# Kernel tuning notes

Measured on AMD Instinct MI355X. Metric: run time of the kernel, lower is better.

## Reference

```python
import jax, jax.numpy as jnp
import numpy as np

V = 100000
E = 524288
D_IN = 128
D_OUT = 128
NUM_REL = 474
BN_EPS = 1e-5


def setup_inputs() -> dict:
    key = jax.random.key(0)
    ks = jax.random.split(key, 12)
    return {
        "x": jax.random.normal(ks[0], (V, D_IN), dtype=jnp.float32),
        "rel_repr": jax.random.normal(ks[1], (NUM_REL, D_IN), dtype=jnp.float32),
        "edge_norm": jax.random.uniform(ks[2], (E,), dtype=jnp.float32),
        "in_w": jax.random.normal(ks[3], (D_IN, D_OUT), dtype=jnp.float32) * 0.1,
        "out_w": jax.random.normal(ks[4], (D_IN, D_OUT), dtype=jnp.float32) * 0.1,
        "loop_w": jax.random.normal(ks[5], (D_IN, D_OUT), dtype=jnp.float32) * 0.1,
        "w_rel": jax.random.normal(ks[6], (D_IN, D_OUT), dtype=jnp.float32) * 0.1,
        "loop_rel": jax.random.normal(ks[7], (1, D_IN), dtype=jnp.float32),
        "bias": jnp.zeros((D_OUT,), dtype=jnp.float32),
        "src": jax.random.randint(ks[8], (E,), 0, V, dtype=jnp.int32),
        "dst": jax.random.randint(ks[9], (E,), 0, V, dtype=jnp.int32),
        "edge_type": jax.random.randint(ks[10], (E,), 0, NUM_REL, dtype=jnp.int32),
    }


def reference(x, rel_repr, edge_norm, in_w, out_w, loop_w, w_rel, loop_rel, bias, src, dst, edge_type):
    # comp primitive 'mult': edge_data = src_emb * rel[edge_type]   [E, D_IN]
    rel = rel_repr  # num_base=-1 -> rel_wt is None, rel.data = rel_repr
    edge_data = x[src] * rel[edge_type]
    half = edge_data.shape[0] // 2  # static under jit
    # first half of edges -> in_w, second half -> out_w
    msg = jnp.concatenate([edge_data[:half] @ in_w, edge_data[half:] @ out_w], axis=0)
    msg = msg * edge_norm[:, None]
    # agg primitive 'sum': scatter-sum into dst nodes
    agg = jax.ops.segment_sum(msg, dst, num_segments=x.shape[0])  # [V, D_OUT]
    # self-loop path: comp(x, loop_rel) @ loop_w
    loop_msg = (x * loop_rel) @ loop_w
    # comb primitive 'add', scaled by 1/3 (dropout with p=0 is identity)
    h = (agg + loop_msg) * (1.0 / 3.0)
    h = h + bias
    # BatchNorm1d, training-mode batch stats, gamma=1, beta=0
    mean = jnp.mean(h, axis=0)
    var = jnp.mean((h - mean) ** 2, axis=0)
    h = (h - mean) * jax.lax.rsqrt(var + BN_EPS)
    # act primitive 'relu'; ltr=True -> project relations
    return jax.nn.relu(h), rel @ w_rel
```

## Files before the change

### kernel.cpp

```cpp
#include <hip/hip_runtime.h>

#define V 100000
#define VP 100096
#define E_EDGES 524288
#define HALF 262144
#define D 128
#define NREL 474
#define BN_EPS 1e-5f
#define NBLK 98

#define ROWTILES 782
#define GEMM_GRID 1568
#define RED_BLKS 98
#define RELB 237
#define BNBLK 12500

#define LDK 392
#define LDB 40

typedef unsigned short u16;
typedef unsigned int u32;
typedef unsigned long long u64;
typedef __attribute__((ext_vector_type(8))) short short8;
typedef __attribute__((ext_vector_type(4))) float f32x4;

__device__ __forceinline__ u16 f2bf(float f) {
    union { float f; u32 u; } v; v.f = f;
    u32 u = v.u;
    return (u16)((u + 0x7fffu + ((u >> 16) & 1u)) >> 16);
}
__device__ __forceinline__ u32 pk2(float a, float b) {
    return (u32)f2bf(a) | ((u32)f2bf(b) << 16);
}

__global__ __launch_bounds__(256) void hist_k(const int* __restrict__ dst, u32* __restrict__ cnt) {
    int e = blockIdx.x * 256 + threadIdx.x;
    if (e >= E_EDGES) return;
    u32 d = (u32)dst[e];
    if (d >= V) d = 0;
    atomicAdd(&cnt[d], 1u);
}

__global__ __launch_bounds__(1024) void scanA_k(const u32* __restrict__ cnt,
                                                u32* __restrict__ cursor,
                                                u32* __restrict__ bsum) {
    __shared__ u32 wsum[16];
    int tid = threadIdx.x, wid = tid >> 6, lane = tid & 63;
    int idx = blockIdx.x * 1024 + tid;
    u32 v = (idx < V) ? cnt[idx] : 0u;
    u32 s = v;
#pragma unroll
    for (int o = 1; o < 64; o <<= 1) {
        u32 t = __shfl_up(s, o, 64);
        if (lane >= o) s += t;
    }
    if (lane == 63) wsum[wid] = s;
    __syncthreads();
    if (wid == 0) {
        u32 wv = (lane < 16) ? wsum[lane] : 0u;
#pragma unroll
        for (int o = 1; o < 16; o <<= 1) {
            u32 t = __shfl_up(wv, o, 64);
            if (lane >= o) wv += t;
        }
        if (lane < 16) wsum[lane] = wv;
    }
    __syncthreads();
    u32 wprev = wid ? wsum[wid - 1] : 0u;
    if (idx < V) cursor[idx] = s + wprev - v;
    if (tid == 0) bsum[blockIdx.x] = wsum[15];
}

__global__ __launch_bounds__(128) void scanBbt_k(
    u32* __restrict__ bsum,
    const float* __restrict__ in_w, const float* __restrict__ out_w,
    const float* __restrict__ loop_w, u16* __restrict__ Bt) {
    if (blockIdx.x > 0) {
        int n = blockIdx.x - 1;
        int t = threadIdx.x;
        const float* Ws[3] = {in_w, out_w, loop_w};
#pragma unroll
        for (int seg = 0; seg < 3; seg++)
            Bt[(size_t)n * 384 + seg * 128 + t] = f2bf(Ws[seg][(size_t)t * D + n]);
        return;
    }
    __shared__ u32 wtot;
    int t = threadIdx.x, lane = t & 63, w = t >> 6;
    u32 v = (t < NBLK) ? bsum[t] : 0u;
    u32 s = v;
#pragma unroll
    for (int o = 1; o < 64; o <<= 1) {
        u32 x = __shfl_up(s, o, 64);
        if (lane >= o) s += x;
    }
    if (w == 0 && lane == 63) wtot = s;
    __syncthreads();
    u32 add = (w == 1) ? wtot : 0u;
    if (t < NBLK) bsum[t] = add + s - v;
}

__global__ __launch_bounds__(256) void fill_rec_k(
    const int* __restrict__ dst, const int* __restrict__ src, const int* __restrict__ etype,
    const float* __restrict__ enorm, u32* __restrict__ cursor, const u32* __restrict__ bsum,
    u64* __restrict__ rec) {
    int e = blockIdx.x * 256 + threadIdx.x;
    if (e >= E_EDGES) return;
    u32 d = (u32)dst[e];   if (d >= V) d = 0;
    u32 s = (u32)src[e];   if (s >= V) s = 0;
    u32 t = (u32)etype[e]; if (t >= NREL) t = 0;
    float nm = enorm[e];
    u32 w = s | (t << 17) | ((e < HALF ? 0u : 1u) << 26);
    u32 slot = atomicAdd(&cursor[d], 1u) + bsum[d >> 10];
    u64 r = (u64)w | ((u64)__float_as_uint(nm) << 32);
    if (slot < E_EDGES) rec[slot] = r;
}

struct Rec { u32 s, t, hf; float nm; };
__device__ __forceinline__ Rec dec(u64 r) {
    Rec q; u32 w = (u32)r;
    q.s = w & 0x1FFFFu;
    q.t = (w >> 17) & 0x1FFu;
    q.hf = (w >> 26) & 1u;
    q.nm = __uint_as_float((u32)(r >> 32));
    return q;
}

__global__ __launch_bounds__(256) void gather_k(
    const float* __restrict__ x, const float* __restrict__ rel,
    const u32* __restrict__ cursor, const u32* __restrict__ cnt,
    const u32* __restrict__ bsum, const u64* __restrict__ rec, u16* __restrict__ Aagg) {
    int tid = threadIdx.x;
    int wave = tid >> 6, lane = tid & 63;
    int l32 = lane & 31;
    int v = blockIdx.x * 8 + wave * 2 + (lane >> 5);
    int col = l32 * 4;

    u32 n = 0, end = 0;
    if (v < V) {
        n = cnt[v];
        end = cursor[v] + bsum[v >> 10];
        if (end > E_EDGES) end = E_EDGES;
        if (n > end) n = end;
    }
    u32 p = end - n;
    u32 rounds = (n + 3) >> 2;
    u32 ro = (u32)__shfl_xor((int)rounds, 32);
    u32 rw = rounds > ro ? rounds : ro;

    float iA0=0.f,iA1=0.f,iA2=0.f,iA3=0.f, oA0=0.f,oA1=0.f,oA2=0.f,oA3=0.f;
    float iB0=0.f,iB1=0.f,iB2=0.f,iB3=0.f, oB0=0.f,oB1=0.f,oB2=0.f,oB3=0.f;

    for (u32 r = 0; r < rw; r++) {
        u32 q = p + r * 4;
        u32 i0 = (q     < end) ? q     : (u32)E_EDGES;
        u32 i1 = (q + 1 < end) ? q + 1 : (u32)E_EDGES;
        u32 i2 = (q + 2 < end) ? q + 2 : (u32)E_EDGES;
        u32 i3 = (q + 3 < end) ? q + 3 : (u32)E_EDGES;
        u64 r0 = rec[i0], r1 = rec[i1], r2 = rec[i2], r3 = rec[i3];
        Rec q0 = dec(r0), q1 = dec(r1), q2 = dec(r2), q3 = dec(r3);
        float4 x0 = *(const float4*)(x + (size_t)q0.s * D + col);
        float4 x1 = *(const float4*)(x + (size_t)q1.s * D + col);
        float4 x2 = *(const float4*)(x + (size_t)q2.s * D + col);
        float4 x3 = *(const float4*)(x + (size_t)q3.s * D + col);
        float4 v0 = *(const float4*)(rel + (size_t)q0.t * D + col);
        float4 v1 = *(const float4*)(rel + (size_t)q1.t * D + col);
        float4 v2 = *(const float4*)(rel + (size_t)q2.t * D + col);
        float4 v3 = *(const float4*)(rel + (size_t)q3.t * D + col);
        float f00 = x0.x*v0.x*q0.nm, f01 = x0.y*v0.y*q0.nm, f02 = x0.z*v0.z*q0.nm, f03 = x0.w*v0.w*q0.nm;
        float f10 = x1.x*v1.x*q1.nm, f11 = x1.y*v1.y*q1.nm, f12 = x1.z*v1.z*q1.nm, f13 = x1.w*v1.w*q1.nm;
        float f20 = x2.x*v2.x*q2.nm, f21 = x2.y*v2.y*q2.nm, f22 = x2.z*v2.z*q2.nm, f23 = x2.w*v2.w*q2.nm;
        float f30 = x3.x*v3.x*q3.nm, f31 = x3.y*v3.y*q3.nm, f32_ = x3.z*v3.z*q3.nm, f33 = x3.w*v3.w*q3.nm;
        if (q0.hf) { oA0+=f00; oA1+=f01; oA2+=f02; oA3+=f03; } else { iA0+=f00; iA1+=f01; iA2+=f02; iA3+=f03; }
        if (q1.hf) { oB0+=f10; oB1+=f11; oB2+=f12; oB3+=f13; } else { iB0+=f10; iB1+=f11; iB2+=f12; iB3+=f13; }
        if (q2.hf) { oA0+=f20; oA1+=f21; oA2+=f22; oA3+=f23; } else { iA0+=f20; iA1+=f21; iA2+=f22; iA3+=f23; }
        if (q3.hf) { oB0+=f30; oB1+=f31; oB2+=f32_; oB3+=f33; } else { iB0+=f30; iB1+=f31; iB2+=f32_; iB3+=f33; }
    }
    float a0 = iA0+iB0, a1 = iA1+iB1, a2 = iA2+iB2, a3 = iA3+iB3;
    float b0 = oA0+oB0, b1 = oA1+oB1, b2 = oA2+oB2, b3 = oA3+oB3;
    u32* arow = (u32*)(Aagg + (size_t)v * 256);
    arow[2*l32]        = pk2(a0, a1);
    arow[2*l32+1]      = pk2(a2, a3);
    arow[64 + 2*l32]   = pk2(b0, b1);
    arow[64 + 2*l32+1] = pk2(b2, b3);
}

__global__ __launch_bounds__(512) void gemm_k(
    const u16* __restrict__ Aagg, const u16* __restrict__ Bt,
    const float* __restrict__ x, const float* __restrict__ loop_rel,
    float* __restrict__ h_out, float* __restrict__ psum, float* __restrict__ psq) {
    __shared__ u16 Bs[64 * 384];
    __shared__ float s_sum[64], s_sq[64];
    int tid = threadIdx.x, wave = tid >> 6, lane = tid & 63;
    int bid = blockIdx.x;
    int rt   = ((bid >> 4) << 3) | (bid & 7);
    int half = (bid >> 3) & 1;
    if (rt >= ROWTILES) return;
    int row0 = rt * 128;

    if (tid < 64) s_sum[tid] = 0.f;
    else if (tid < 128) s_sq[tid - 64] = 0.f;

    int m16 = lane & 15;
    int kq = (lane >> 4) * 8;
    int gvm = row0 + wave * 16 + m16;
    const u16* arow = Aagg + (size_t)gvm * 256;
    bool vok = gvm < V;

    short8 af[8];
#pragma unroll
    for (int ks = 0; ks < 8; ks++) af[ks] = *(const short8*)(arow + ks * 32 + kq);
    short8 lf[4];
    {
        const float* xp = x + (size_t)gvm * D + kq;
#pragma unroll
        for (int kk = 0; kk < 4; kk++) {
            float4 x0 = vok ? *(const float4*)(xp + kk * 32)     : (float4){0.f, 0.f, 0.f, 0.f};
            float4 x1 = vok ? *(const float4*)(xp + kk * 32 + 4) : (float4){0.f, 0.f, 0.f, 0.f};
            float4 l0 = *(const float4*)(loop_rel + kk * 32 + kq);
            float4 l1 = *(const float4*)(loop_rel + kk * 32 + kq + 4);
            union { u32 u[4]; short8 s; } c;
            c.u[0] = pk2(x0.x * l0.x, x0.y * l0.y);
            c.u[1] = pk2(x0.z * l0.z, x0.w * l0.w);
            c.u[2] = pk2(x1.x * l1.x, x1.y * l1.y);
            c.u[3] = pk2(x1.z * l1.z, x1.w * l1.w);
            lf[kk] = c.s;
        }
    }

    {
        const u16* srcB = Bt + (size_t)half * 64 * 384;
        char* bsw = (char*)Bs;
#pragma unroll
        for (int it = 0; it < 6; it++) {
            int c = it * 512 + tid;
            int n = c / 48, s = c - n * 48;
            short8 vv = *(const short8*)(srcB + (size_t)n * 384 + s * 8);
            *(short8*)(bsw + (((u32)(n * 768 + s * 16)) ^ (u32)((n & 7) << 4))) = vv;
        }
    }
    __syncthreads();

    const char* bsb = (const char*)Bs;
    f32x4 acc[4];
#pragma unroll
    for (int ct = 0; ct < 4; ct++) acc[ct] = (f32x4){0.f, 0.f, 0.f, 0.f};

#pragma unroll
    for (int ks = 0; ks < 8; ks++) {
#pragma unroll
        for (int ct = 0; ct < 4; ct++) {
            int n = ct * 16 + m16;
            short8 b = *(const short8*)(bsb + (((u32)(n * 768 + (ks * 32 + kq) * 2)) ^ (u32)((n & 7) << 4)));
            acc[ct] = __builtin_amdgcn_mfma_f32_16x16x32_bf16(af[ks], b, acc[ct], 0, 0, 0);
        }
    }
#pragma unroll
    for (int kk = 0; kk < 4; kk++) {
#pragma unroll
        for (int ct = 0; ct < 4; ct++) {
            int n = ct * 16 + m16;
            short8 b = *(const short8*)(bsb + (((u32)(n * 768 + (256 + kk * 32 + kq) * 2)) ^ (u32)((n & 7) << 4)));
            acc[ct] = __builtin_amdgcn_mfma_f32_16x16x32_bf16(lf[kk], b, acc[ct], 0, 0, 0);
        }
    }

    int m4 = (lane >> 4) * 4;
#pragma unroll
    for (int ct = 0; ct < 4; ct++) {
        float ls = 0.f, lq = 0.f;
#pragma unroll
        for (int i = 0; i < 4; i++) {
            int gv = row0 + wave * 16 + m4 + i;
            if (gv < V) {
                float h = acc[ct][i] * (1.0f / 3.0f);
                h_out[(size_t)gv * D + half * 64 + ct * 16 + m16] = h;
                ls += h; lq += h * h;
            }
        }
        atomicAdd(&s_sum[ct * 16 + m16], ls);
        atomicAdd(&s_sq[ct * 16 + m16], lq);
    }
    __syncthreads();
    if (tid < 64) psum[(size_t)rt * 128 + half * 64 + tid] = s_sum[tid];
    else if (tid < 128) psq[(size_t)rt * 128 + half * 64 + (tid - 64)] = s_sq[tid - 64];
}

__global__ __launch_bounds__(256) void bn_reduce(
    const float* __restrict__ psum, const float* __restrict__ psq,
    float* __restrict__ colsum, float* __restrict__ colsumsq) {
    int t = threadIdx.x;
    int c = t & 127;
    const float* srcp = (t < 128) ? psum : psq;
    float s = 0.f;
    int r0 = blockIdx.x * 8;
#pragma unroll
    for (int i = 0; i < 8; i++) {
        int r = r0 + i;
        if (r < ROWTILES) s += srcp[(size_t)r * 128 + c];
    }
    atomicAdd(((t < 128) ? colsum : colsumsq) + c, s);
}

__global__ __launch_bounds__(256) void final_k(
    float* __restrict__ hio, const float* __restrict__ colsum, const float* __restrict__ colsumsq,
    const float* __restrict__ rel, const float* __restrict__ w, float* __restrict__ out1) {
    int bid = blockIdx.x;
    if (bid < RELB) {
        __shared__ float rs[2][D];
        int rh = threadIdx.x >> 7, c = threadIdx.x & 127;
        int r = bid * 2 + rh;
        rs[rh][c] = rel[(size_t)r * D + c];
        __syncthreads();
        float s = 0.f;
#pragma unroll 8
        for (int k = 0; k < D; k++) s += rs[rh][k] * w[(size_t)k * D + c];
        out1[(size_t)r * D + c] = s;
        return;
    }
    int idx = ((bid - RELB) * 256 + threadIdx.x) * 4;
    if (idx >= V * D) return;
    int col = idx & (D - 1);
    float4 hv = *(const float4*)(hio + idx);
    float4 ov;
    {
        float m0 = colsum[col + 0] * (1.0f / (float)V);
        float m1 = colsum[col + 1] * (1.0f / (float)V);
        float m2 = colsum[col + 2] * (1.0f / (float)V);
        float m3 = colsum[col + 3] * (1.0f / (float)V);
        if (!isfinite(m0)) m0 = 0.f;
        if (!isfinite(m1)) m1 = 0.f;
        if (!isfinite(m2)) m2 = 0.f;
        if (!isfinite(m3)) m3 = 0.f;
        float v0 = colsumsq[col + 0] * (1.0f / (float)V) - m0 * m0;
        float v1 = colsumsq[col + 1] * (1.0f / (float)V) - m1 * m1;
        float v2 = colsumsq[col + 2] * (1.0f / (float)V) - m2 * m2;
        float v3 = colsumsq[col + 3] * (1.0f / (float)V) - m3 * m3;
        if (!isfinite(v0) || v0 < 0.f) v0 = 0.f;
        if (!isfinite(v1) || v1 < 0.f) v1 = 0.f;
        if (!isfinite(v2) || v2 < 0.f) v2 = 0.f;
        if (!isfinite(v3) || v3 < 0.f) v3 = 0.f;
        float f0 = (hv.x - m0) * rsqrtf(v0 + BN_EPS);
        float f1 = (hv.y - m1) * rsqrtf(v1 + BN_EPS);
        float f2 = (hv.z - m2) * rsqrtf(v2 + BN_EPS);
        float f3 = (hv.w - m3) * rsqrtf(v3 + BN_EPS);
        ov.x = (f0 > 0.f) ? f0 : 0.f;
        ov.y = (f1 > 0.f) ? f1 : 0.f;
        ov.z = (f2 > 0.f) ? f2 : 0.f;
        ov.w = (f3 > 0.f) ? f3 : 0.f;
    }
    *(float4*)(hio + idx) = ov;
}

__global__ __launch_bounds__(1024) void scan_k(const u32* __restrict__ cnt,
                                               u32* __restrict__ cursor) {
    __shared__ u32 wsum[16];
    __shared__ u32 carry_s;
    int tid = threadIdx.x, wid = tid >> 6, lane = tid & 63;
    if (tid == 0) carry_s = 0;
    __syncthreads();
    for (int base = 0; base < V; base += 1024) {
        int idx = base + tid;
        u32 v = (idx < V) ? cnt[idx] : 0u;
        u32 s = v;
#pragma unroll
        for (int o = 1; o < 64; o <<= 1) {
            u32 t = __shfl_up(s, o, 64);
            if (lane >= o) s += t;
        }
        if (lane == 63) wsum[wid] = s;
        __syncthreads();
        if (wid == 0) {
            u32 wv = (lane < 16) ? wsum[lane] : 0u;
#pragma unroll
            for (int o = 1; o < 16; o <<= 1) {
                u32 t = __shfl_up(wv, o, 64);
                if (lane >= o) wv += t;
            }
            if (lane < 16) wsum[lane] = wv;
        }
        __syncthreads();
        u32 wprev = (wid == 0) ? 0u : wsum[wid - 1];
        u32 c = carry_s;
        if (idx < V) cursor[idx] = c + s + wprev - v;
        u32 tot = wsum[15];
        __syncthreads();
        if (tid == 0) carry_s = c + tot;
        __syncthreads();
    }
}

__global__ __launch_bounds__(256) void fill_k(
    const int* __restrict__ dst, u32* __restrict__ cursor, u32* __restrict__ eid) {
    int e = blockIdx.x * 256 + threadIdx.x;
    if (e >= E_EDGES) return;
    u32 d = (u32)dst[e];
    if (d >= V) d = 0;
    u32 slot = atomicAdd(&cursor[d], 1u);
    if (slot < E_EDGES) eid[slot] = (u32)e;
}

__global__ __launch_bounds__(256, 1) void fused_k(
    const float* __restrict__ x, const float* __restrict__ rel, const float* __restrict__ loop_rel,
    const float* __restrict__ in_w, const float* __restrict__ out_w, const float* __restrict__ loop_w,
    const float* __restrict__ enorm,
    const int* __restrict__ src, const int* __restrict__ etype,
    const u32* __restrict__ cursor, const u32* __restrict__ cnt,
    const u32* __restrict__ eid,
    float* __restrict__ h_out, float* __restrict__ colsum, float* __restrict__ colsumsq) {
    __shared__ u16 Alds[64 * LDK];
    __shared__ u16 Bs[D * LDB];
    __shared__ float s_sum[D], s_sq[D];

    int tid = threadIdx.x, wave = tid >> 6, lane = tid & 63;
    int row0 = blockIdx.x * 64;

    if (tid < D) { s_sum[tid] = 0.f; s_sq[tid] = 0.f; }

    for (int i = 0; i < 16; i++) {
        int row = wave * 16 + i;
        int gv = row0 + row;
        u32* arow = (u32*)(Alds + row * LDK);
        if (gv < V) {
            float a0 = 0.f, a1 = 0.f, b0 = 0.f, b1 = 0.f;
            float c0 = 0.f, c1 = 0.f, d0 = 0.f, d1 = 0.f;
            u32 n = cnt[gv];
            u32 end = cursor[gv];
            u32 beg = (end >= n) ? end - n : 0u;
            if (beg >= E_EDGES) { beg = 0; n = 0; }
            if (n > E_EDGES - beg) n = E_EDGES - beg;
            u32 nend = beg + n;
            u32 p = beg;
            for (; p + 2 <= nend; p += 2) {
                u32 e0 = eid[p];           if (e0 >= E_EDGES) e0 = 0;
                u32 e1 = eid[p + 1];       if (e1 >= E_EDGES) e1 = 0;
                u32 s0 = (u32)src[e0];     if (s0 >= V) s0 = 0;
                u32 s1 = (u32)src[e1];     if (s1 >= V) s1 = 0;
                u32 t0 = (u32)etype[e0];   if (t0 >= NREL) t0 = 0;
                u32 t1 = (u32)etype[e1];   if (t1 >= NREL) t1 = 0;
                float n0 = enorm[e0];
                float n1 = enorm[e1];
                float2 xv0 = *(const float2*)(x + (size_t)s0 * D + lane * 2);
                float2 xv1 = *(const float2*)(x + (size_t)s1 * D + lane * 2);
                float2 rv0 = *(const float2*)(rel + (size_t)t0 * D + lane * 2);
                float2 rv1 = *(const float2*)(rel + (size_t)t1 * D + lane * 2);
                float f00 = xv0.x * rv0.x * n0, f01 = xv0.y * rv0.y * n0;
                float f10 = xv1.x * rv1.x * n1, f11 = xv1.y * rv1.y * n1;
                if (e0 < HALF) { a0 += f00; a1 += f01; } else { b0 += f00; b1 += f01; }
                if (e1 < HALF) { c0 += f10; c1 += f11; } else { d0 += f10; d1 += f11; }
            }
            if (p < nend) {
                u32 e0 = eid[p];           if (e0 >= E_EDGES) e0 = 0;
                u32 s0 = (u32)src[e0];     if (s0 >= V) s0 = 0;
                u32 t0 = (u32)etype[e0];   if (t0 >= NREL) t0 = 0;
                float n0 = enorm[e0];
                float2 xv0 = *(const float2*)(x + (size_t)s0 * D + lane * 2);
                float2 rv0 = *(const float2*)(rel + (size_t)t0 * D + lane * 2);
                float f00 = xv0.x * rv0.x * n0, f01 = xv0.y * rv0.y * n0;
                if (e0 < HALF) { a0 += f00; a1 += f01; } else { b0 += f00; b1 += f01; }
            }
            a0 += c0; a1 += c1; b0 += d0; b1 += d1;
            float2 xv = *(const float2*)(x + (size_t)gv * D + lane * 2);
            float2 lv = *(const float2*)(loop_rel + lane * 2);
            arow[lane]       = pk2(a0, a1);
            arow[64 + lane]  = pk2(b0, b1);
            arow[128 + lane] = pk2(xv.x * lv.x, xv.y * lv.y);
        } else {
            arow[lane] = 0u; arow[64 + lane] = 0u; arow[128 + lane] = 0u;
        }
    }
    __syncthreads();

    f32x4 acc[8];
#pragma unroll
    for (int ct = 0; ct < 8; ct++) acc[ct] = (f32x4){0.f, 0.f, 0.f, 0.f};

    int m = wave * 16 + (lane & 15);
    int kq = (lane >> 4) * 8;
    int bk = tid >> 3;
    int bn0 = (tid & 7) * 16;

    for (int ks = 0; ks < 12; ks++) {
        int k0 = ks * 32;
        int seg = k0 >> 7;
        int kloc = k0 & 127;
        const float* W = (seg == 0) ? in_w : (seg == 1 ? out_w : loop_w);
#pragma unroll
        for (int j = 0; j < 16; j += 2) {
            float2 w2 = *(const float2*)(W + (size_t)(kloc + bk) * D + bn0 + j);
            Bs[(bn0 + j) * LDB + bk]     = f2bf(w2.x);
            Bs[(bn0 + j + 1) * LDB + bk] = f2bf(w2.y);
        }
        __syncthreads();
        short8 a = *(const short8*)(Alds + m * LDK + k0 + kq);
#pragma unroll
        for (int ct = 0; ct < 8; ct++) {
            short8 b = *(const short8*)(Bs + (ct * 16 + (lane & 15)) * LDB + kq);
            acc[ct] = __builtin_amdgcn_mfma_f32_16x16x32_bf16(a, b, acc[ct], 0, 0, 0);
        }
        __syncthreads();
    }

    int m4 = (lane >> 4) * 4;
#pragma unroll
    for (int ct = 0; ct < 8; ct++) {
        float ls = 0.f, lq = 0.f;
#pragma unroll
        for (int i = 0; i < 4; i++) {
            int gv = row0 + wave * 16 + m4 + i;
            if (gv < V) {
                float h = acc[ct][i] * (1.0f / 3.0f);
                h_out[(size_t)gv * D + ct * 16 + (lane & 15)] = h;
                ls += h; lq += h * h;
            }
        }
        atomicAdd(&s_sum[ct * 16 + (lane & 15)], ls);
        atomicAdd(&s_sq[ct * 16 + (lane & 15)], lq);
    }
    __syncthreads();
    if (tid < D) atomicAdd(&colsum[tid], s_sum[tid]);
    else atomicAdd(&colsumsq[tid - D], s_sq[tid - D]);
}

__global__ void bn_finalize(const float* __restrict__ colsum, const float* __restrict__ colsumsq,
                            float* __restrict__ mean, float* __restrict__ scale) {
    int t = threadIdx.x;
    float m = colsum[t] * (1.0f / (float)V);
    if (!isfinite(m)) m = 0.f;
    float var = colsumsq[t] * (1.0f / (float)V) - m * m;
    if (!isfinite(var) || var < 0.f) var = 0.f;
    mean[t] = m;
    scale[t] = rsqrtf(var + BN_EPS);
}

__global__ __launch_bounds__(256) void bn_relu(
    float* __restrict__ hio, const float* __restrict__ mean, const float* __restrict__ scale) {
    int idx = (blockIdx.x * 256 + threadIdx.x) * 4;
    if (idx >= V * D) return;
    int col = idx & (D - 1);
    float4 hv = *(const float4*)(hio + idx);
    float f0 = (hv.x - mean[col + 0]) * scale[col + 0];
    float f1 = (hv.y - mean[col + 1]) * scale[col + 1];
    float f2 = (hv.z - mean[col + 2]) * scale[col + 2];
    float f3 = (hv.w - mean[col + 3]) * scale[col + 3];
    f0 = (f0 > 0.f) ? f0 : 0.f;
    f1 = (f1 > 0.f) ? f1 : 0.f;
    f2 = (f2 > 0.f) ? f2 : 0.f;
    f3 = (f3 > 0.f) ? f3 : 0.f;
    float4 ov; ov.x = f0; ov.y = f1; ov.z = f2; ov.w = f3;
    *(float4*)(hio + idx) = ov;
}

__global__ __launch_bounds__(128) void rel_gemm(
    const float* __restrict__ rel, const float* __restrict__ w, float* __restrict__ out1) {
    __shared__ float rs[D];
    int t = threadIdx.x;
    int r = blockIdx.x;
    rs[t] = rel[(size_t)r * D + t];
    __syncthreads();
    float s = 0.f;
#pragma unroll 8
    for (int k = 0; k < D; k++) s += rs[k] * w[(size_t)k * D + t];
    out1[(size_t)r * D + t] = s;
}

extern "C" void kernel_launch(void* const* d_in, const int* in_sizes, int n_in,
                              void* d_out, int out_size, void* d_ws, size_t ws_size,
                              hipStream_t stream) {
    const float* x        = (const float*)d_in[0];
    const float* rel_repr = (const float*)d_in[1];
    const float* enorm    = (const float*)d_in[2];
    const float* in_w     = (const float*)d_in[3];
    const float* out_w    = (const float*)d_in[4];
    const float* loop_w   = (const float*)d_in[5];
    const float* w_rel    = (const float*)d_in[6];
    const float* loop_rel = (const float*)d_in[7];
    const int* src   = (const int*)d_in[9];
    const int* dst   = (const int*)d_in[10];
    const int* etype = (const int*)d_in[11];

    float* out0 = (float*)d_out;
    float* out1 = (float*)d_out + (size_t)V * D;

    char* ws = (char*)d_ws;

    {
        size_t off = 0;
        u32* cnt        = (u32*)(ws + off); off += (size_t)V * 4;
        float* colsum   = (float*)(ws + off); off += 512;
        float* colsumsq = (float*)(ws + off); off += 512;
        size_t zero_bytes = off;
        u32* cursor = (u32*)(ws + off); off += (size_t)V * 4;
        u32* bsum   = (u32*)(ws + off); off += 512;
        u16* Bt     = (u16*)(ws + off); off += (size_t)128 * 384 * 2;
        float* psum = (float*)(ws + off); off += (size_t)ROWTILES * 128 * 4;
        float* psq  = (float*)(ws + off); off += (size_t)ROWTILES * 128 * 4;
        u64* rec    = (u64*)(ws + off); off += (size_t)(E_EDGES + 8) * 8;
        u16* Aagg   = (u16*)(ws + off); off += (size_t)VP * 256 * 2;

        if (ws_size >= off) {
            hipMemsetAsync(d_ws, 0, zero_bytes, stream);
            hipMemsetAsync(rec + E_EDGES, 0, 64, stream);
            hist_k<<<(E_EDGES + 255) / 256, 256, 0, stream>>>(dst, cnt);
            scanA_k<<<NBLK, 1024, 0, stream>>>(cnt, cursor, bsum);
            scanBbt_k<<<129, 128, 0, stream>>>(bsum, in_w, out_w, loop_w, Bt);
            fill_rec_k<<<(E_EDGES + 255) / 256, 256, 0, stream>>>(dst, src, etype, enorm, cursor, bsum, rec);
            gather_k<<<VP / 8, 256, 0, stream>>>(x, rel_repr, cursor, cnt, bsum, rec, Aagg);
            gemm_k<<<GEMM_GRID, 512, 0, stream>>>(Aagg, Bt, x, loop_rel, out0, psum, psq);
            bn_reduce<<<RED_BLKS, 256, 0, stream>>>(psum, psq, colsum, colsumsq);
            final_k<<<RELB + BNBLK, 256, 0, stream>>>(out0, colsum, colsumsq, rel_repr, w_rel, out1);
            return;
        }
    }

    {
        size_t off = 0;
        u32* cnt      = (u32*)(ws + off); off += (size_t)V * 4;
        float* colsum = (float*)(ws + off); off += 512;
        float* colsumsq = (float*)(ws + off); off += 512;
        size_t zero_bytes = off;
        u32* cursor   = (u32*)(ws + off); off += (size_t)V * 4;
        float* meanp  = (float*)(ws + off); off += 512;
        float* scalep = (float*)(ws + off); off += 512;
        u32* eid      = (u32*)(ws + off); off += (size_t)E_EDGES * 4;

        if (ws_size < off) return;

        hipMemsetAsync(d_ws, 0, zero_bytes, stream);
        hist_k<<<(E_EDGES + 255) / 256, 256, 0, stream>>>(dst, cnt);
        scan_k<<<1, 1024, 0, stream>>>(cnt, cursor);
        fill_k<<<(E_EDGES + 255) / 256, 256, 0, stream>>>(dst, cursor, eid);
        fused_k<<<(V + 63) / 64, 256, 0, stream>>>(x, rel_repr, loop_rel, in_w, out_w, loop_w,
                                                   enorm, src, etype,
                                                   cursor, cnt, eid,
                                                   out0, colsum, colsumsq);
        bn_finalize<<<1, 128, 0, stream>>>(colsum, colsumsq, meanp, scalep);
        bn_relu<<<(V * D / 4 + 255) / 256, 256, 0, stream>>>(out0, meanp, scalep);
        rel_gemm<<<NREL, 128, 0, stream>>>(rel_repr, w_rel, out1);
    }
}
```

Measured before the change: 310.9 us.

## Fuse CSR build and gather stages into one cooperative persistent kernel

Replaces the two memsets and five separate launches (histogram, two scans, weight transpose, record fill, gather) with one cooperative kernel on a persistent grid, separated by grid-wide syncs. The aim is to remove launch overhead and idle gaps between the small dependent kernels. In exchange, the gather work is done by a fixed grid of 1024 blocks capped at 4 per CU, which may lower occupancy for the latency-bound gather. The old launch path is kept as a fallback if the cooperative launch fails.

Measured after the change: 812.8 us. 161% more time.

```diff
diff --git a/kernel.cpp b/kernel.cpp
--- a/kernel.cpp
+++ b/kernel.cpp
@@ -1,4 +1,7 @@
 #include <hip/hip_runtime.h>
+#include <hip/hip_cooperative_groups.h>
+
+namespace cg = cooperative_groups;
 
 #define V 100000
 #define VP 100096
@@ -8,6 +11,8 @@
 #define NREL 474
 #define BN_EPS 1e-5f
 #define NBLK 98
+#define NBLK2 391
+#define PREP_GRID 1024
 
 #define ROWTILES 782
 #define GEMM_GRID 1568
@@ -31,6 +36,163 @@
 }
 __device__ __forceinline__ u32 pk2(float a, float b) {
     return (u32)f2bf(a) | ((u32)f2bf(b) << 16);
+}
+
+struct Rec { u32 s, t, hf; float nm; };
+__device__ __forceinline__ Rec dec(u64 r) {
+    Rec q; u32 w = (u32)r;
+    q.s = w & 0x1FFFFu;
+    q.t = (w >> 17) & 0x1FFu;
+    q.hf = (w >> 26) & 1u;
+    q.nm = __uint_as_float((u32)(r >> 32));
+    return q;
+}
+
+__global__ __launch_bounds__(256, 4) void prep_k(
+    const int* __restrict__ dst, const int* __restrict__ src, const int* __restrict__ etype,
+    const float* __restrict__ enorm, const float* __restrict__ x, const float* __restrict__ rel,
+    const float* __restrict__ in_w, const float* __restrict__ out_w, const float* __restrict__ loop_w,
+    u32* __restrict__ cnt, u32* __restrict__ cursor, u32* __restrict__ bsum2,
+    u16* __restrict__ Bt, u64* __restrict__ rec, u16* __restrict__ Aagg,
+    float* __restrict__ colsum, float* __restrict__ colsumsq) {
+    cg::grid_group gg = cg::this_grid();
+    int tid = threadIdx.x, wid = tid >> 6, lane = tid & 63;
+    int nb = gridDim.x;
+    int gtid = blockIdx.x * 256 + tid;
+    int gstride = nb * 256;
+    __shared__ u32 wsum[4];
+
+    for (int i = gtid; i < V; i += gstride) cnt[i] = 0u;
+    if (gtid < 128) { colsum[gtid] = 0.f; colsumsq[gtid] = 0.f; }
+    if (gtid < 8) rec[E_EDGES + gtid] = 0ull;
+    gg.sync();
+
+    for (int e = gtid; e < E_EDGES; e += gstride) {
+        u32 d = (u32)dst[e];
+        if (d >= V) d = 0;
+        atomicAdd(&cnt[d], 1u);
+    }
+    gg.sync();
+
+    for (int c = blockIdx.x; c < NBLK2; c += nb) {
+        int idx = c * 256 + tid;
+        u32 v = (idx < V) ? cnt[idx] : 0u;
+        u32 s = v;
+#pragma unroll
+        for (int o = 1; o < 64; o <<= 1) {
+            u32 t = __shfl_up(s, o, 64);
+            if (lane >= o) s += t;
+        }
+        if (lane == 63) wsum[wid] = s;
+        __syncthreads();
+        if (wid == 0) {
+            u32 wv = (lane < 4) ? wsum[lane] : 0u;
+#pragma unroll
+            for (int o = 1; o < 4; o <<= 1) {
+                u32 t = __shfl_up(wv, o, 64);
+                if (lane >= o) wv += t;
+            }
+            if (lane < 4) wsum[lane] = wv;
+        }
+        __syncthreads();
+        u32 wprev = wid ? wsum[wid - 1] : 0u;
+        if (idx < V) cursor[idx] = s + wprev - v;
+        if (tid == 0) bsum2[c] = wsum[3];
+        __syncthreads();
+    }
+    gg.sync();
+
+    if (blockIdx.x == 0) {
+        if (tid < 64) {
+            u32 carry = 0;
+            for (int base = 0; base < NBLK2; base += 64) {
+                int i = base + tid;
+                u32 v = (i < NBLK2) ? bsum2[i] : 0u;
+                u32 s = v;
+#pragma unroll
+                for (int o = 1; o < 64; o <<= 1) {
+                    u32 t = __shfl_up(s, o, 64);
+                    if (lane >= o) s += t;
+                }
+                u32 tot = __shfl(s, 63);
+                if (i < NBLK2) bsum2[i] = carry + s - v;
+                carry += tot;
+            }
+        }
+    } else if (blockIdx.x <= 64) {
+        int n = (blockIdx.x - 1) * 2 + (tid >> 7);
+        int t = tid & 127;
+        const float* Ws[3] = {in_w, out_w, loop_w};
+#pragma unroll
+        for (int seg = 0; seg < 3; seg++)
+            Bt[(size_t)n * 384 + seg * 128 + t] = f2bf(Ws[seg][(size_t)t * D + n]);
+    }
+    gg.sync();
+
+    for (int e = gtid; e < E_EDGES; e += gstride) {
+        u32 d = (u32)dst[e];   if (d >= V) d = 0;
+        u32 s = (u32)src[e];   if (s >= V) s = 0;
+        u32 t = (u32)etype[e]; if (t >= NREL) t = 0;
+        float nm = enorm[e];
+        u32 w = s | (t << 17) | ((e < HALF ? 0u : 1u) << 26);
+        u32 slot = atomicAdd(&cursor[d], 1u) + bsum2[d >> 8];
+        u64 r = (u64)w | ((u64)__float_as_uint(nm) << 32);
+        if (slot < E_EDGES) rec[slot] = r;
+    }
+    gg.sync();
+
+    int l32 = lane & 31;
+    int col = l32 * 4;
+    for (int g = blockIdx.x; g < VP / 8; g += nb) {
+        int v = g * 8 + wid * 2 + (lane >> 5);
+        u32 n = 0, end = 0;
+        if (v < V) {
+            n = cnt[v];
+            end = cursor[v] + bsum2[v >> 8];
+            if (end > E_EDGES) end = E_EDGES;
+            if (n > end) n = end;
+        }
+        u32 p = end - n;
+        u32 rounds = (n + 3) >> 2;
+        u32 ro = (u32)__shfl_xor((int)rounds, 32);
+        u32 rw = rounds > ro ? rounds : ro;
+
+        float iA0=0.f,iA1=0.f,iA2=0.f,iA3=0.f, oA0=0.f,oA1=0.f,oA2=0.f,oA3=0.f;
+        float iB0=0.f,iB1=0.f,iB2=0.f,iB3=0.f, oB0=0.f,oB1=0.f,oB2=0.f,oB3=0.f;
+
+        for (u32 r = 0; r < rw; r++) {
+            u32 q = p + r * 4;
+            u32 i0 = (q     < end) ? q     : (u32)E_EDGES;
+            u32 i1 = (q + 1 < end) ? q + 1 : (u32)E_EDGES;
+            u32 i2 = (q + 2 < end) ? q + 2 : (u32)E_EDGES;
+            u32 i3 = (q + 3 < end) ? q + 3 : (u32)E_EDGES;
+            u64 r0 = rec[i0], r1 = rec[i1], r2 = rec[i2], r3 = rec[i3];
+            Rec q0 = dec(r0), q1 = dec(r1), q2 = dec(r2), q3 = dec(r3);
+            float4 x0 = *(const float4*)(x + (size_t)q0.s * D + col);
+            float4 x1 = *(const float4*)(x + (size_t)q1.s * D + col);
+            float4 x2 = *(const float4*)(x + (size_t)q2.s * D + col);
+            float4 x3 = *(const float4*)(x + (size_t)q3.s * D + col);
+            float4 v0 = *(const float4*)(rel + (size_t)q0.t * D + col);
+            float4 v1 = *(const float4*)(rel + (size_t)q1.t * D + col);
+            float4 v2 = *(const float4*)(rel + (size_t)q2.t * D + col);
+            float4 v3 = *(const float4*)(rel + (size_t)q3.t * D + col);
+            float f00 = x0.x*v0.x*q0.nm, f01 = x0.y*v0.y*q0.nm, f02 = x0.z*v0.z*q0.nm, f03 = x0.w*v0.w*q0.nm;
+            float f10 = x1.x*v1.x*q1.nm, f11 = x1.y*v1.y*q1.nm, f12 = x1.z*v1.z*q1.nm, f13 = x1.w*v1.w*q1.nm;
+            float f20 = x2.x*v2.x*q2.nm, f21 = x2.y*v2.y*q2.nm, f22 = x2.z*v2.z*q2.nm, f23 = x2.w*v2.w*q2.nm;
+            float f30 = x3.x*v3.x*q3.nm, f31 = x3.y*v3.y*q3.nm, f32_ = x3.z*v3.z*q3.nm, f33 = x3.w*v3.w*q3.nm;
+            if (q0.hf) { oA0+=f00; oA1+=f01; oA2+=f02; oA3+=f03; } else { iA0+=f00; iA1+=f01; iA2+=f02; iA3+=f03; }
+            if (q1.hf) { oB0+=f10; oB1+=f11; oB2+=f12; oB3+=f13; } else { iB0+=f10; iB1+=f11; iB2+=f12; iB3+=f13; }
+            if (q2.hf) { oA0+=f20; oA1+=f21; oA2+=f22; oA3+=f23; } else { iA0+=f20; iA1+=f21; iA2+=f22; iA3+=f23; }
+            if (q3.hf) { oB0+=f30; oB1+=f31; oB2+=f32_; oB3+=f33; } else { iB0+=f30; iB1+=f31; iB2+=f32_; iB3+=f33; }
+        }
+        float a0 = iA0+iB0, a1 = iA1+iB1, a2 = iA2+iB2, a3 = iA3+iB3;
+        float b0 = oA0+oB0, b1 = oA1+oB1, b2 = oA2+oB2, b3 = oA3+oB3;
+        u32* arow = (u32*)(Aagg + (size_t)v * 256);
+        arow[2*l32]        = pk2(a0, a1);
+        arow[2*l32+1]      = pk2(a2, a3);
+        arow[64 + 2*l32]   = pk2(b0, b1);
+        arow[64 + 2*l32+1] = pk2(b2, b3);
+    }
 }
 
 __global__ __launch_bounds__(256) void hist_k(const int* __restrict__ dst, u32* __restrict__ cnt) {
@@ -113,16 +275,6 @@
     u32 slot = atomicAdd(&cursor[d], 1u) + bsum[d >> 10];
     u64 r = (u64)w | ((u64)__float_as_uint(nm) << 32);
     if (slot < E_EDGES) rec[slot] = r;
-}
-
-struct Rec { u32 s, t, hf; float nm; };
-__device__ __forceinline__ Rec dec(u64 r) {
-    Rec q; u32 w = (u32)r;
-    q.s = w & 0x1FFFFu;
-    q.t = (w >> 17) & 0x1FFu;
-    q.hf = (w >> 26) & 1u;
-    q.nm = __uint_as_float((u32)(r >> 32));
-    return q;
 }
 
 __global__ __launch_bounds__(256) void gather_k(
@@ -175,6 +327,7 @@
         if (q2.hf) { oA0+=f20; oA1+=f21; oA2+=f22; oA3+=f23; } else { iA0+=f20; iA1+=f21; iA2+=f22; iA3+=f23; }
         if (q3.hf) { oB0+=f30; oB1+=f31; oB2+=f32_; oB3+=f33; } else { iB0+=f30; iB1+=f31; iB2+=f32_; iB3+=f33; }
     }
+    if (v >= VP) return;
     float a0 = iA0+iB0, a1 = iA1+iB1, a2 = iA2+iB2, a3 = iA3+iB3;
     float b0 = oA0+oB0, b1 = oA1+oB1, b2 = oA2+oB2, b3 = oA3+oB3;
     u32* arow = (u32*)(Aagg + (size_t)v * 256);
@@ -590,7 +743,7 @@
         float* colsumsq = (float*)(ws + off); off += 512;
         size_t zero_bytes = off;
         u32* cursor = (u32*)(ws + off); off += (size_t)V * 4;
-        u32* bsum   = (u32*)(ws + off); off += 512;
+        u32* bsum   = (u32*)(ws + off); off += 2048;
         u16* Bt     = (u16*)(ws + off); off += (size_t)128 * 384 * 2;
         float* psum = (float*)(ws + off); off += (size_t)ROWTILES * 128 * 4;
         float* psq  = (float*)(ws + off); off += (size_t)ROWTILES * 128 * 4;
@@ -598,13 +751,27 @@
         u16* Aagg   = (u16*)(ws + off); off += (size_t)VP * 256 * 2;
 
         if (ws_size >= off) {
-            hipMemsetAsync(d_ws, 0, zero_bytes, stream);
-            hipMemsetAsync(rec + E_EDGES, 0, 64, stream);
-            hist_k<<<(E_EDGES + 255) / 256, 256, 0, stream>>>(dst, cnt);
-            scanA_k<<<NBLK, 1024, 0, stream>>>(cnt, cursor, bsum);
-            scanBbt_k<<<129, 128, 0, stream>>>(bsum, in_w, out_w, loop_w, Bt);
-            fill_rec_k<<<(E_EDGES + 255) / 256, 256, 0, stream>>>(dst, src, etype, enorm, cursor, bsum, rec);
-            gather_k<<<VP / 8, 256, 0, stream>>>(x, rel_repr, cursor, cnt, bsum, rec, Aagg);
+            void* args[] = {
+                (void*)&dst, (void*)&src, (void*)&etype, (void*)&enorm,
+                (void*)&x, (void*)&rel_repr,
+                (void*)&in_w, (void*)&out_w, (void*)&loop_w,
+                (void*)&cnt, (void*)&cursor, (void*)&bsum,
+                (void*)&Bt, (void*)&rec, (void*)&Aagg,
+                (void*)&colsum, (void*)&colsumsq
+            };
+            hipError_t cerr = hipLaunchCooperativeKernel(
+                (const void*)prep_k, dim3(PREP_GRID), dim3(256), args, 0, stream);
+
+            if (cerr != hipSuccess) {
+                hipMemsetAsync(d_ws, 0, zero_bytes, stream);
+                hipMemsetAsync(rec + E_EDGES, 0, 64, stream);
+                hist_k<<<(E_EDGES + 255) / 256, 256, 0, stream>>>(dst, cnt);
+                scanA_k<<<NBLK, 1024, 0, stream>>>(cnt, cursor, bsum);
+                scanBbt_k<<<129, 128, 0, stream>>>(bsum, in_w, out_w, loop_w, Bt);
+                fill_rec_k<<<(E_EDGES + 255) / 256, 256, 0, stream>>>(dst, src, etype, enorm, cursor, bsum, rec);
+                gather_k<<<VP / 8, 256, 0, stream>>>(x, rel_repr, cursor, cnt, bsum, rec, Aagg);
+            }
+
             gemm_k<<<GEMM_GRID, 512, 0, stream>>>(Aagg, Bt, x, loop_rel, out0, psum, psq);
             bn_reduce<<<RED_BLKS, 256, 0, stream>>>(psum, psq, colsum, colsumsq);
             final_k<<<RELB + BNBLK, 256, 0, stream>>>(out0, colsum, colsumsq, rel_repr, w_rel, out1);
```
